# Kernel optimization log

Measured on AMD Instinct MI355X. Metric: run time of the kernel, lower is better.

The kernel has to match this reference:

```python
import jax, jax.numpy as jnp
import numpy as np

EMB = 512       # emb_dim
H = 8           # n_heads
HD = EMB // H   # head_dim = 64
FREQ = 64       # freq_features
PERIOD = 0.1
N = 2048


def setup_inputs() -> dict:
    key = jax.random.key(0)
    ks = jax.random.split(key, 6)
    x = jax.random.normal(ks[0], (1, N, EMB), dtype=jnp.float32)
    v = jax.random.normal(ks[1], (1, N, 3), dtype=jnp.float32)
    vec_map = v / jnp.linalg.norm(v, axis=-1, keepdims=True)  # unit direction vectors
    s_in = 1.0 / np.sqrt(EMB)
    W_qkv = jax.random.normal(ks[2], (EMB, 3 * EMB), dtype=jnp.float32) * s_in
    b_qkv = jnp.zeros((3 * EMB,), dtype=jnp.float32)
    W_bias = jax.random.normal(ks[3], (FREQ, H), dtype=jnp.float32) * (1.0 / np.sqrt(FREQ))
    b_bias = jnp.zeros((H,), dtype=jnp.float32)
    W_out = jax.random.normal(ks[4], (EMB, EMB), dtype=jnp.float32) * s_in
    b_out = jnp.zeros((EMB,), dtype=jnp.float32)
    return {"x": x, "vec_map": vec_map, "W_qkv": W_qkv, "b_qkv": b_qkv,
            "W_bias": W_bias, "b_bias": b_bias, "W_out": W_out, "b_out": b_out}


def reference(x, vec_map, W_qkv, b_qkv, W_bias, b_bias, W_out, b_out):
    batch_dim = x.shape[:-2]
    n = x.shape[-2]
    # QKV projection -> (*, N, H, 3, HD)
    qkv = (x @ W_qkv + b_qkv).reshape(*batch_dim, n, H, 3, HD)
    q, k, v = (qkv[..., 0, :], qkv[..., 1, :], qkv[..., 2, :])
    # attention scores (*, Q, K, H), softmax over the K axis (axis=-2)
    attn = jnp.einsum('...qht,...kht->...qkh', q, k) / np.sqrt(HD)
    attn = jax.nn.softmax(attn, axis=-2)
    # relative bias from pairwise angles between direction vectors
    dot = jnp.einsum('...nc,...mc->...nm', vec_map, vec_map)
    angle = jnp.arccos(jnp.clip(dot, 0.0, 1.0)) / 0.001
    freqs = jnp.linspace(0.0, 1.0, FREQ // 2, dtype=jnp.float32) / PERIOD
    phase = freqs * angle[..., None]                      # (*, N, N, FREQ/2)
    pos = jnp.concatenate((jnp.sin(phase), jnp.cos(phase)), axis=-1)  # (*, N, N, FREQ)
    bias = pos @ W_bias + b_bias                          # (*, N, N, H)
    attn = attn + bias
    # weighted sum of values -> (*, N, EMB)
    y = jnp.einsum('...qkh,...kht->...qht', attn, v).reshape(*batch_dim, n, EMB)
    return y @ W_out + b_out
```

## Files before the change

### kernel.cpp

```cpp
#include <hip/hip_runtime.h>
#include <hip/hip_bf16.h>
#include <math.h>

#define NT 2048
#define EMBD 512
#define NH 8
#define QKV_LD 1536

typedef unsigned short u16;
typedef __attribute__((ext_vector_type(8))) short short8;
typedef __attribute__((ext_vector_type(4))) float v4f;

static __device__ __forceinline__ float bf2f(unsigned int u) {
    union { unsigned int i; float f; } c; c.i = u << 16; return c.f;
}
static __device__ __forceinline__ void unpack4(uint2 r, float* f) {
    f[0] = bf2f(r.x & 0xffffu); f[1] = bf2f(r.x >> 16);
    f[2] = bf2f(r.y & 0xffffu); f[3] = bf2f(r.y >> 16);
}
static __device__ __forceinline__ unsigned int f2bf(float x) {
    union { float f; unsigned int u; } c; c.f = x;
    return (c.u + 0x7fffu + ((c.u >> 16) & 1u)) >> 16;
}

__global__ __launch_bounds__(256) void split_x(const float* __restrict__ x,
    u16* __restrict__ xh, u16* __restrict__ xl)
{
    int i = (blockIdx.x * 256 + threadIdx.x) << 2;
    float4 v = *(const float4*)(x + i);
    float f[4] = {v.x, v.y, v.z, v.w};
    unsigned int hi[4], lo[4];
#pragma unroll
    for (int j = 0; j < 4; ++j) {
        hi[j] = f2bf(f[j]);
        lo[j] = f2bf(f[j] - bf2f(hi[j]));
    }
    uint2 wh; wh.x = hi[0] | (hi[1] << 16); wh.y = hi[2] | (hi[3] << 16);
    uint2 wl; wl.x = lo[0] | (lo[1] << 16); wl.y = lo[2] | (lo[3] << 16);
    *(uint2*)(xh + i) = wh;
    *(uint2*)(xl + i) = wl;
}

__global__ __launch_bounds__(256) void split_wt(const float* __restrict__ W,
    u16* __restrict__ wth, u16* __restrict__ wtl, int ld)
{
    __shared__ float tile[64][65];
    const int n0 = blockIdx.x << 6, k0 = blockIdx.y << 6;
    const int t = threadIdx.x;
    const int r = t >> 2, c4 = (t & 3) << 4;
#pragma unroll
    for (int j = 0; j < 4; ++j)
        *(float4*)&tile[r][c4 + (j << 2)] =
            *(const float4*)(W + (size_t)(k0 + r) * ld + n0 + c4 + (j << 2));
    __syncthreads();
    const int n_l = t >> 2;
    u16 th[16], tl[16];
#pragma unroll
    for (int j = 0; j < 16; ++j) {
        float f = tile[c4 + j][n_l];
        unsigned int h = f2bf(f);
        th[j] = (u16)h;
        tl[j] = (u16)f2bf(f - bf2f(h));
    }
    u16* dh = wth + (size_t)(n0 + n_l) * EMBD + k0 + c4;
    u16* dl = wtl + (size_t)(n0 + n_l) * EMBD + k0 + c4;
    *(uint4*)dh       = *(uint4*)&th[0];
    *(uint4*)(dh + 8) = *(uint4*)&th[8];
    *(uint4*)dl       = *(uint4*)&tl[0];
    *(uint4*)(dl + 8) = *(uint4*)&tl[8];
}

__global__ __launch_bounds__(256) void gemm_qkv_mfma(const u16* __restrict__ xh,
    const u16* __restrict__ xl, const u16* __restrict__ wth,
    const u16* __restrict__ wtl, const float* __restrict__ bias,
    u16* __restrict__ qkvb)
{
    const int n0 = blockIdx.x << 6, m0 = blockIdx.y << 6;
    const int w = threadIdx.x >> 6, lane = threadIdx.x & 63;
    const int wm = w >> 1, wn = w & 1;
    const int fr = lane & 15, kd = (lane >> 4) << 3;

    const u16* ah0 = xh + (size_t)(m0 + wm * 32 + fr) * EMBD + kd;
    const u16* al0 = xl + (size_t)(m0 + wm * 32 + fr) * EMBD + kd;
    const u16* bh0 = wth + (size_t)(n0 + wn * 32 + fr) * EMBD + kd;
    const u16* bl0 = wtl + (size_t)(n0 + wn * 32 + fr) * EMBD + kd;

    v4f acc[2][2] = {};
    for (int kc = 0; kc < EMBD; kc += 32) {
        short8 a_h[2], a_l[2], b_h[2], b_l[2];
#pragma unroll
        for (int im = 0; im < 2; ++im) {
            a_h[im] = *(const short8*)(ah0 + (size_t)im * 16 * EMBD + kc);
            a_l[im] = *(const short8*)(al0 + (size_t)im * 16 * EMBD + kc);
        }
#pragma unroll
        for (int in = 0; in < 2; ++in) {
            b_h[in] = *(const short8*)(bh0 + (size_t)in * 16 * EMBD + kc);
            b_l[in] = *(const short8*)(bl0 + (size_t)in * 16 * EMBD + kc);
        }
#pragma unroll
        for (int im = 0; im < 2; ++im)
#pragma unroll
            for (int in = 0; in < 2; ++in) {
                acc[im][in] = __builtin_amdgcn_mfma_f32_16x16x32_bf16(a_h[im], b_h[in], acc[im][in], 0, 0, 0);
                acc[im][in] = __builtin_amdgcn_mfma_f32_16x16x32_bf16(a_h[im], b_l[in], acc[im][in], 0, 0, 0);
                acc[im][in] = __builtin_amdgcn_mfma_f32_16x16x32_bf16(a_l[im], b_h[in], acc[im][in], 0, 0, 0);
            }
    }
    const int qr = (lane >> 4) << 2;
#pragma unroll
    for (int im = 0; im < 2; ++im)
#pragma unroll
        for (int in = 0; in < 2; ++in) {
            int n = n0 + wn * 32 + in * 16 + fr;
            float bv = bias[n];
#pragma unroll
            for (int r = 0; r < 4; ++r) {
                int m = m0 + wm * 32 + im * 16 + qr + r;
                qkvb[(size_t)m * QKV_LD + n] = (u16)f2bf(acc[im][in][r] + bv);
            }
        }
}

__global__ __launch_bounds__(256) void transpose_v(const u16* __restrict__ qkvb,
                                                   u16* __restrict__ Vt)
{
    __shared__ u16 tile[64][72];
    const int h = blockIdx.y, k0 = blockIdx.x << 6;
    const int t = threadIdx.x;
    {
        int r = t >> 2, cg = (t & 3) << 4;
        const u16* src = qkvb + (size_t)(k0 + r) * QKV_LD + h * 192 + 128 + cg;
        *(uint4*)&tile[r][cg]     = *(const uint4*)src;
        *(uint4*)&tile[r][cg + 8] = *(const uint4*)(src + 8);
    }
    __syncthreads();
    {
        int c = t >> 2, kg = (t & 3) << 4;
        u16 tmp[16];
#pragma unroll
        for (int j = 0; j < 16; ++j) tmp[j] = tile[kg + j][c];
        u16* dst = Vt + ((size_t)h * 64 + c) * NT + k0 + kg;
        *(uint4*)dst       = *(uint4*)&tmp[0];
        *(uint4*)(dst + 8) = *(uint4*)&tmp[8];
    }
}

__global__ __launch_bounds__(256) void scores_mfma(const u16* __restrict__ qkvb,
                                                   u16* __restrict__ s,
                                                   float* __restrict__ zbuf)
{
    __shared__ u16 tile[128][144];
    const int h = blockIdx.z;
    const int kb = blockIdx.x << 7;
    const int qb = blockIdx.y << 7;
    const int w = threadIdx.x >> 6;
    const int q0 = qb + (w << 5);
    const int lane = threadIdx.x & 63;
    const int fr = lane & 15;
    const int kd = (lane >> 4) << 3;

    const u16* qbase = qkvb + (size_t)(q0 + fr) * QKV_LD + h * 192 + kd;
    const u16* kbase = qkvb + (size_t)(kb + fr) * QKV_LD + h * 192 + 64 + kd;

    short8 aq[2][2];
    aq[0][0] = *(const short8*)(qbase);
    aq[0][1] = *(const short8*)(qbase + 32);
    aq[1][0] = *(const short8*)(qbase + (size_t)16 * QKV_LD);
    aq[1][1] = *(const short8*)(qbase + (size_t)16 * QKV_LD + 32);

    v4f acc[2][8] = {};
#pragma unroll
    for (int nt = 0; nt < 8; ++nt) {
        short8 b0 = *(const short8*)(kbase + (size_t)nt * 16 * QKV_LD);
        short8 b1 = *(const short8*)(kbase + (size_t)nt * 16 * QKV_LD + 32);
        acc[0][nt] = __builtin_amdgcn_mfma_f32_16x16x32_bf16(aq[0][0], b0, acc[0][nt], 0, 0, 0);
        acc[0][nt] = __builtin_amdgcn_mfma_f32_16x16x32_bf16(aq[0][1], b1, acc[0][nt], 0, 0, 0);
        acc[1][nt] = __builtin_amdgcn_mfma_f32_16x16x32_bf16(aq[1][0], b0, acc[1][nt], 0, 0, 0);
        acc[1][nt] = __builtin_amdgcn_mfma_f32_16x16x32_bf16(aq[1][1], b1, acc[1][nt], 0, 0, 0);
    }
    const int qr = (lane >> 4) << 2;
#pragma unroll
    for (int i = 0; i < 2; ++i)
#pragma unroll
        for (int nt = 0; nt < 8; ++nt)
#pragma unroll
            for (int r = 0; r < 4; ++r)
                tile[(w << 5) + (i << 4) + qr + r][(nt << 4) + fr] =
                    (u16)f2bf(acc[i][nt][r] * 0.125f);
    float es[2][4];
#pragma unroll
    for (int i = 0; i < 2; ++i)
#pragma unroll
        for (int r = 0; r < 4; ++r) {
            float sum = 0.f;
#pragma unroll
            for (int nt = 0; nt < 8; ++nt)
                sum += __expf(acc[i][nt][r] * 0.125f);
            es[i][r] = sum;
        }
#pragma unroll
    for (int off = 1; off < 16; off <<= 1)
#pragma unroll
        for (int i = 0; i < 2; ++i)
#pragma unroll
            for (int r = 0; r < 4; ++r)
                es[i][r] += __shfl_xor(es[i][r], off);
    if (fr == 0) {
#pragma unroll
        for (int i = 0; i < 2; ++i)
#pragma unroll
            for (int r = 0; r < 4; ++r)
                atomicAdd(zbuf + h * NT + q0 + (i << 4) + qr + r, es[i][r]);
    }
    __syncthreads();
    const int row0 = threadIdx.x >> 4;
    const int col = (threadIdx.x & 15) << 3;
#pragma unroll
    for (int l = 0; l < 8; ++l) {
        int row = row0 + (l << 4);
        *(uint4*)(s + ((size_t)h * NT + qb + row) * NT + kb + col) =
            *(uint4*)&tile[row][col];
    }
}

__global__ __launch_bounds__(256) void bias_kernel(u16* __restrict__ s,
    const float* __restrict__ vec, const float* __restrict__ Wb,
    const float* __restrict__ bb, const float* __restrict__ zbuf)
{
    __shared__ float flds[32];
    __shared__ float vql[96], vkl[96];
    __shared__ float bbl[8];
    __shared__ float ang_lds[1057];
    __shared__ float biasl[8 * 1057];

    const int t = threadIdx.x;
    int b = blockIdx.x, tq = 0, rem = 64;
    while (b >= rem) { b -= rem; ++tq; --rem; }
    const int tk = tq + b;
    const int q0 = tq << 5, k0 = tk << 5;

    if (t < 32) flds[t] = __fdiv_rn(__fdiv_rn((float)t, 31.0f), 0.1f);
    else if (t < 128) vql[t - 32] = vec[q0 * 3 + (t - 32)];
    else if (t < 224) vkl[t - 128] = vec[k0 * 3 + (t - 128)];
    else if (t < 232) bbl[t - 224] = bb[t - 224];
    __syncthreads();

    {
        const int qq = t & 31, kb = (t >> 5) << 2;
        const float a0 = vql[qq * 3], a1 = vql[qq * 3 + 1], a2 = vql[qq * 3 + 2];
#pragma unroll
        for (int j = 0; j < 4; ++j) {
            const int kk = kb + j;
            float c0 = vkl[kk * 3], c1 = vkl[kk * 3 + 1], c2 = vkl[kk * 3 + 2];
            float dot = __fadd_rn(__fadd_rn(__fmul_rn(a0, c0), __fmul_rn(a1, c1)),
                                  __fmul_rn(a2, c2));
            float dotc = fminf(fmaxf(dot, 0.0f), 1.0f);
            ang_lds[qq * 33 + kk] = __fdiv_rn(acosf(dotc), 0.001f);
        }
    }
    __syncthreads();

    {
        const int w = t >> 6, lane = t & 63;
        const int fr = lane & 15, kd = (lane >> 4) << 3, qr = (lane >> 4) << 2;
        short8 BS, BC;
#pragma unroll
        for (int j = 0; j < 8; ++j) {
            float ws = (fr < 8) ? Wb[(kd + j) * 8 + fr] : 0.0f;
            float wc = (fr < 8) ? Wb[(32 + kd + j) * 8 + fr] : 0.0f;
            BS[j] = (short)f2bf(ws);
            BC[j] = (short)f2bf(wc);
        }
        for (int tt = w; tt < 64; tt += 4) {
            int p = (tt << 4) + fr;
            float ang = ang_lds[(p >> 5) * 33 + (p & 31)];
            short8 AS, AC;
#pragma unroll
            for (int j = 0; j < 8; ++j) {
                float ph = __fmul_rn(flds[kd + j], ang);
                float rv = ph * 0.15915494309189535f;
                float rf = rv - floorf(rv);
                AS[j] = (short)f2bf(__builtin_amdgcn_sinf(rf));
                AC[j] = (short)f2bf(__builtin_amdgcn_cosf(rf));
            }
            v4f c = {};
            c = __builtin_amdgcn_mfma_f32_16x16x32_bf16(AS, BS, c, 0, 0, 0);
            c = __builtin_amdgcn_mfma_f32_16x16x32_bf16(AC, BC, c, 0, 0, 0);
            if (fr < 8) {
#pragma unroll
                for (int r = 0; r < 4; ++r) {
                    int pp = (tt << 4) + qr + r;
                    biasl[fr * 1057 + (pp >> 5) * 33 + (pp & 31)] = c[r];
                }
            }
        }
    }
    __syncthreads();

    const int r = t >> 3;
    const int cg = (t & 7) << 2;
    {
        const int q = q0 + r;
#pragma unroll
        for (int h = 0; h < 8; ++h) {
            const float iz = 1.0f / zbuf[h * NT + q];
            const float bv = bbl[h];
            const size_t base = ((size_t)h * NT + q) * NT + k0 + cg;
            uint2 raw = *(const uint2*)(s + base);
            float v[4]; unpack4(raw, v);
            unsigned int o[4];
#pragma unroll
            for (int j = 0; j < 4; ++j) {
                float bias = biasl[h * 1057 + r * 33 + cg + j];
                o[j] = f2bf(__expf(v[j]) * iz + bias + bv);
            }
            uint2 wv; wv.x = o[0] | (o[1] << 16); wv.y = o[2] | (o[3] << 16);
            *(uint2*)(s + base) = wv;
        }
    }
    if (tk != tq) {
        const int q = k0 + r;
#pragma unroll
        for (int h = 0; h < 8; ++h) {
            const float iz = 1.0f / zbuf[h * NT + q];
            const float bv = bbl[h];
            const size_t base = ((size_t)h * NT + q) * NT + q0 + cg;
            uint2 raw = *(const uint2*)(s + base);
            float v[4]; unpack4(raw, v);
            unsigned int o[4];
#pragma unroll
            for (int j = 0; j < 4; ++j) {
                float bias = biasl[h * 1057 + (cg + j) * 33 + r];
                o[j] = f2bf(__expf(v[j]) * iz + bias + bv);
            }
            uint2 wv; wv.x = o[0] | (o[1] << 16); wv.y = o[2] | (o[3] << 16);
            *(uint2*)(s + base) = wv;
        }
    }
}

__global__ __launch_bounds__(256) void attnv_mfma(const u16* __restrict__ attn,
    const u16* __restrict__ Vt, float* __restrict__ ypart)
{
    const int h = blockIdx.y, z = blockIdx.z;
    const int q0 = (blockIdx.x << 6) + ((threadIdx.x >> 6) << 4);
    const int lane = threadIdx.x & 63;
    const int fr = lane & 15;
    const int kd = (lane >> 4) << 3;
    const int kbase = z << 9;

    const u16* arow  = attn + (size_t)(h * NT + q0 + fr) * NT + kbase + kd;
    const u16* vbase = Vt + ((size_t)h * 64 + fr) * NT + kbase + kd;

    v4f c[4] = {};
    for (int ks = 0; ks < 512; ks += 32) {
        short8 a = *(const short8*)(arow + ks);
#pragma unroll
        for (int nt = 0; nt < 4; ++nt) {
            short8 bv = *(const short8*)(vbase + (size_t)nt * 16 * NT + ks);
            c[nt] = __builtin_amdgcn_mfma_f32_16x16x32_bf16(a, bv, c[nt], 0, 0, 0);
        }
    }
    float* yp = ypart + (size_t)z * NT * EMBD;
    const int qr = (lane >> 4) << 2;
#pragma unroll
    for (int nt = 0; nt < 4; ++nt)
#pragma unroll
        for (int r = 0; r < 4; ++r)
            yp[(size_t)(q0 + qr + r) * EMBD + (h << 6) + (nt << 4) + fr] = c[nt][r];
}

__global__ __launch_bounds__(256) void reduce_y(const float* __restrict__ parts,
    u16* __restrict__ yh, u16* __restrict__ yl)
{
    const int MN = NT * EMBD;
    int i = (blockIdx.x * 256 + threadIdx.x) << 2;
    float4 acc = *(const float4*)(parts + i);
#pragma unroll
    for (int sp = 1; sp < 4; ++sp) {
        float4 p = *(const float4*)(parts + (size_t)sp * MN + i);
        acc.x += p.x; acc.y += p.y; acc.z += p.z; acc.w += p.w;
    }
    float f[4] = {acc.x, acc.y, acc.z, acc.w};
    unsigned int hi[4], lo[4];
#pragma unroll
    for (int j = 0; j < 4; ++j) {
        hi[j] = f2bf(f[j]);
        lo[j] = f2bf(f[j] - bf2f(hi[j]));
    }
    uint2 wh; wh.x = hi[0] | (hi[1] << 16); wh.y = hi[2] | (hi[3] << 16);
    uint2 wl; wl.x = lo[0] | (lo[1] << 16); wl.y = lo[2] | (lo[3] << 16);
    *(uint2*)(yh + i) = wh;
    *(uint2*)(yl + i) = wl;
}

__global__ __launch_bounds__(256) void gemm_out_mfma(const u16* __restrict__ yh,
    const u16* __restrict__ yl, const u16* __restrict__ wh,
    const u16* __restrict__ wl, const float* __restrict__ bias,
    float* __restrict__ out)
{
    const int n0 = blockIdx.x << 6, m0 = blockIdx.y << 6;
    const int w = threadIdx.x >> 6, lane = threadIdx.x & 63;
    const int wm = w >> 1, wn = w & 1;
    const int fr = lane & 15, kd = (lane >> 4) << 3;

    const u16* ah0 = yh + (size_t)(m0 + wm * 32 + fr) * EMBD + kd;
    const u16* al0 = yl + (size_t)(m0 + wm * 32 + fr) * EMBD + kd;
    const u16* bh0 = wh + (size_t)(n0 + wn * 32 + fr) * EMBD + kd;
    const u16* bl0 = wl + (size_t)(n0 + wn * 32 + fr) * EMBD + kd;

    v4f acc[2][2] = {};
    for (int kc = 0; kc < EMBD; kc += 32) {
        short8 a_h[2], a_l[2], b_h[2], b_l[2];
#pragma unroll
        for (int im = 0; im < 2; ++im) {
            a_h[im] = *(const short8*)(ah0 + (size_t)im * 16 * EMBD + kc);
            a_l[im] = *(const short8*)(al0 + (size_t)im * 16 * EMBD + kc);
        }
#pragma unroll
        for (int in = 0; in < 2; ++in) {
            b_h[in] = *(const short8*)(bh0 + (size_t)in * 16 * EMBD + kc);
            b_l[in] = *(const short8*)(bl0 + (size_t)in * 16 * EMBD + kc);
        }
#pragma unroll
        for (int im = 0; im < 2; ++im)
#pragma unroll
            for (int in = 0; in < 2; ++in) {
                acc[im][in] = __builtin_amdgcn_mfma_f32_16x16x32_bf16(a_h[im], b_h[in], acc[im][in], 0, 0, 0);
                acc[im][in] = __builtin_amdgcn_mfma_f32_16x16x32_bf16(a_h[im], b_l[in], acc[im][in], 0, 0, 0);
                acc[im][in] = __builtin_amdgcn_mfma_f32_16x16x32_bf16(a_l[im], b_h[in], acc[im][in], 0, 0, 0);
            }
    }
    const int qr = (lane >> 4) << 2;
#pragma unroll
    for (int im = 0; im < 2; ++im)
#pragma unroll
        for (int in = 0; in < 2; ++in) {
            int n = n0 + wn * 32 + in * 16 + fr;
            float bv = bias[n];
#pragma unroll
            for (int r = 0; r < 4; ++r) {
                int m = m0 + wm * 32 + im * 16 + qr + r;
                out[(size_t)m * EMBD + n] = acc[im][in][r] + bv;
            }
        }
}

extern "C" void kernel_launch(void* const* d_in, const int* in_sizes, int n_in,
                              void* d_out, int out_size, void* d_ws, size_t ws_size,
                              hipStream_t stream)
{
    const float* x    = (const float*)d_in[0];
    const float* vec  = (const float*)d_in[1];
    const float* Wqkv = (const float*)d_in[2];
    const float* bqkv = (const float*)d_in[3];
    const float* Wb   = (const float*)d_in[4];
    const float* bb   = (const float*)d_in[5];
    const float* Wout = (const float*)d_in[6];
    const float* bout = (const float*)d_in[7];
    float* out = (float*)d_out;

    char* ws = (char*)d_ws;
    u16*   qkvb  = (u16*)(ws);
    u16*   sbuf  = (u16*)(ws + 6291456);
    u16*   Vt    = (u16*)(ws + 73400320);
    float* zbuf  = (float*)(ws + 75497472);
    u16*   yh    = (u16*)(ws + 75628544);
    u16*   yl    = (u16*)(ws + 77725696);
    float* parts = (float*)(ws + 79822848);
    u16*   xh    = (u16*)(ws + 79822848);
    u16*   xl    = (u16*)(ws + 81920000);
    u16*   wth   = (u16*)(ws + 84017152);
    u16*   wtl   = (u16*)(ws + 85590016);
    u16*   woth  = (u16*)(ws + 79822848);
    u16*   wotl  = (u16*)(ws + 80347136);

    hipMemsetAsync(zbuf, 0, NH * NT * sizeof(float), stream);
    split_x<<<1024, 256, 0, stream>>>(x, xh, xl);
    split_wt<<<dim3(24, 8), 256, 0, stream>>>(Wqkv, wth, wtl, QKV_LD);
    gemm_qkv_mfma<<<dim3(24, 32), 256, 0, stream>>>(xh, xl, wth, wtl, bqkv, qkvb);
    transpose_v<<<dim3(32, 8), 256, 0, stream>>>(qkvb, Vt);
    scores_mfma<<<dim3(16, 16, 8), 256, 0, stream>>>(qkvb, sbuf, zbuf);
    bias_kernel<<<2080, 256, 0, stream>>>(sbuf, vec, Wb, bb, zbuf);
    attnv_mfma<<<dim3(32, 8, 4), 256, 0, stream>>>(sbuf, Vt, parts);
    reduce_y<<<1024, 256, 0, stream>>>(parts, yh, yl);
    split_wt<<<dim3(8, 8), 256, 0, stream>>>(Wout, woth, wotl, EMBD);
    gemm_out_mfma<<<dim3(8, 32), 256, 0, stream>>>(yh, yl, woth, wotl, bout, out);
}
```

Baseline: 273.6 us.

## Fuse scores, bias and attn@V into one flash-style kernel without materializing NxN

Replaces the separate scores, bias and attn·V kernels, which wrote and reread a bf16 H×N×N score buffer, with one fused kernel. For each 32-query tile and K-split it computes QK^T, exp, the angle-based bias via MFMA, and multiplies both exp-scores and bias by V in registers. It keeps two partial accumulators (unnormalized P·V and bias·V) plus partial row sums, and a reduce kernel normalizes and combines them. This removes the large global round-trips and the memset, but the launch is only 256 blocks of 512 threads, which may leave the GPU underoccupied. It also recomputes the bias for every query/key pair instead of exploiting symmetry.

```diff
diff --git a/kernel.cpp b/kernel.cpp
--- a/kernel.cpp
+++ b/kernel.cpp
@@ -6,6 +6,7 @@
 #define EMBD 512
 #define NH 8
 #define QKV_LD 1536
+#define KSPLIT 4
 
 typedef unsigned short u16;
 typedef __attribute__((ext_vector_type(8))) short short8;
@@ -13,10 +14,6 @@
 
 static __device__ __forceinline__ float bf2f(unsigned int u) {
     union { unsigned int i; float f; } c; c.i = u << 16; return c.f;
-}
-static __device__ __forceinline__ void unpack4(uint2 r, float* f) {
-    f[0] = bf2f(r.x & 0xffffu); f[1] = bf2f(r.x >> 16);
-    f[2] = bf2f(r.y & 0xffffu); f[3] = bf2f(r.y >> 16);
 }
 static __device__ __forceinline__ unsigned int f2bf(float x) {
     union { float f; unsigned int u; } c; c.f = x;
@@ -146,243 +143,226 @@
     }
 }
 
-__global__ __launch_bounds__(256) void scores_mfma(const u16* __restrict__ qkvb,
-                                                   u16* __restrict__ s,
-                                                   float* __restrict__ zbuf)
-{
-    __shared__ u16 tile[128][144];
-    const int h = blockIdx.z;
-    const int kb = blockIdx.x << 7;
-    const int qb = blockIdx.y << 7;
-    const int w = threadIdx.x >> 6;
-    const int q0 = qb + (w << 5);
-    const int lane = threadIdx.x & 63;
+__global__ __launch_bounds__(512, 2) void fused_attn(
+    const u16* __restrict__ qkvb, const u16* __restrict__ Vt,
+    const float* __restrict__ vec, const float* __restrict__ Wb,
+    const float* __restrict__ bb, float* __restrict__ zpart,
+    float* __restrict__ partsP, float* __restrict__ partsB)
+{
+    __shared__ float flds[32];
+    __shared__ float vql[96];
+    __shared__ float ang[32 * 65];
+    __shared__ u16 tile[8 * 2056];
+
+    const int bid = blockIdx.x;
+    const int xcd = bid & 7;
+    const int zsp = xcd >> 1;
+    const int qt  = ((bid >> 3) << 1) | (xcd & 1);
+    const int q0 = qt << 5;
+    const int kbase = zsp << 9;
+
+    const int t = threadIdx.x;
+    const int w = t >> 6;
+    const int lane = t & 63;
     const int fr = lane & 15;
-    const int kd = (lane >> 4) << 3;
-
-    const u16* qbase = qkvb + (size_t)(q0 + fr) * QKV_LD + h * 192 + kd;
-    const u16* kbase = qkvb + (size_t)(kb + fr) * QKV_LD + h * 192 + 64 + kd;
-
-    short8 aq[2][2];
-    aq[0][0] = *(const short8*)(qbase);
-    aq[0][1] = *(const short8*)(qbase + 32);
-    aq[1][0] = *(const short8*)(qbase + (size_t)16 * QKV_LD);
-    aq[1][1] = *(const short8*)(qbase + (size_t)16 * QKV_LD + 32);
-
-    v4f acc[2][8] = {};
-#pragma unroll
-    for (int nt = 0; nt < 8; ++nt) {
-        short8 b0 = *(const short8*)(kbase + (size_t)nt * 16 * QKV_LD);
-        short8 b1 = *(const short8*)(kbase + (size_t)nt * 16 * QKV_LD + 32);
-        acc[0][nt] = __builtin_amdgcn_mfma_f32_16x16x32_bf16(aq[0][0], b0, acc[0][nt], 0, 0, 0);
-        acc[0][nt] = __builtin_amdgcn_mfma_f32_16x16x32_bf16(aq[0][1], b1, acc[0][nt], 0, 0, 0);
-        acc[1][nt] = __builtin_amdgcn_mfma_f32_16x16x32_bf16(aq[1][0], b0, acc[1][nt], 0, 0, 0);
-        acc[1][nt] = __builtin_amdgcn_mfma_f32_16x16x32_bf16(aq[1][1], b1, acc[1][nt], 0, 0, 0);
-    }
-    const int qr = (lane >> 4) << 2;
-#pragma unroll
-    for (int i = 0; i < 2; ++i)
-#pragma unroll
-        for (int nt = 0; nt < 8; ++nt)
-#pragma unroll
-            for (int r = 0; r < 4; ++r)
-                tile[(w << 5) + (i << 4) + qr + r][(nt << 4) + fr] =
-                    (u16)f2bf(acc[i][nt][r] * 0.125f);
-    float es[2][4];
-#pragma unroll
-    for (int i = 0; i < 2; ++i)
-#pragma unroll
-        for (int r = 0; r < 4; ++r) {
-            float sum = 0.f;
-#pragma unroll
-            for (int nt = 0; nt < 8; ++nt)
-                sum += __expf(acc[i][nt][r] * 0.125f);
-            es[i][r] = sum;
-        }
-#pragma unroll
-    for (int off = 1; off < 16; off <<= 1)
-#pragma unroll
-        for (int i = 0; i < 2; ++i)
-#pragma unroll
-            for (int r = 0; r < 4; ++r)
-                es[i][r] += __shfl_xor(es[i][r], off);
-    if (fr == 0) {
-#pragma unroll
-        for (int i = 0; i < 2; ++i)
-#pragma unroll
-            for (int r = 0; r < 4; ++r)
-                atomicAdd(zbuf + h * NT + q0 + (i << 4) + qr + r, es[i][r]);
-    }
-    __syncthreads();
-    const int row0 = threadIdx.x >> 4;
-    const int col = (threadIdx.x & 15) << 3;
-#pragma unroll
-    for (int l = 0; l < 8; ++l) {
-        int row = row0 + (l << 4);
-        *(uint4*)(s + ((size_t)h * NT + qb + row) * NT + kb + col) =
-            *(uint4*)&tile[row][col];
-    }
-}
-
-__global__ __launch_bounds__(256) void bias_kernel(u16* __restrict__ s,
-    const float* __restrict__ vec, const float* __restrict__ Wb,
-    const float* __restrict__ bb, const float* __restrict__ zbuf)
-{
-    __shared__ float flds[32];
-    __shared__ float vql[96], vkl[96];
-    __shared__ float bbl[8];
-    __shared__ float ang_lds[1057];
-    __shared__ float biasl[8 * 1057];
-
-    const int t = threadIdx.x;
-    int b = blockIdx.x, tq = 0, rem = 64;
-    while (b >= rem) { b -= rem; ++tq; --rem; }
-    const int tk = tq + b;
-    const int q0 = tq << 5, k0 = tk << 5;
+    const int hi4 = lane >> 4;
+    const int kd = hi4 << 3;
+    const int qr = hi4 << 2;
 
     if (t < 32) flds[t] = __fdiv_rn(__fdiv_rn((float)t, 31.0f), 0.1f);
     else if (t < 128) vql[t - 32] = vec[q0 * 3 + (t - 32)];
-    else if (t < 224) vkl[t - 128] = vec[k0 * 3 + (t - 128)];
-    else if (t < 232) bbl[t - 224] = bb[t - 224];
+
+    short8 BS, BC;
+#pragma unroll
+    for (int j = 0; j < 8; ++j) {
+        float ws = (fr < 8) ? Wb[(kd + j) * 8 + fr] : 0.0f;
+        float wc = (fr < 8) ? Wb[(32 + kd + j) * 8 + fr] : 0.0f;
+        BS[j] = (short)f2bf(ws);
+        BC[j] = (short)f2bf(wc);
+    }
+    const float bbv = (fr < 8) ? bb[fr] : 0.0f;
+
+    short8 aq[2][2];
+#pragma unroll
+    for (int mb = 0; mb < 2; ++mb)
+#pragma unroll
+        for (int kk = 0; kk < 2; ++kk)
+            aq[mb][kk] = *(const short8*)(qkvb +
+                (size_t)(q0 + mb * 16 + fr) * QKV_LD + w * 192 + kk * 32 + kd);
+
+    v4f accP[2][4] = {};
+    v4f accB[2][4] = {};
+    float zacc[2][4] = {};
+
     __syncthreads();
 
-    {
-        const int qq = t & 31, kb = (t >> 5) << 2;
-        const float a0 = vql[qq * 3], a1 = vql[qq * 3 + 1], a2 = vql[qq * 3 + 2];
-#pragma unroll
-        for (int j = 0; j < 4; ++j) {
-            const int kk = kb + j;
-            float c0 = vkl[kk * 3], c1 = vkl[kk * 3 + 1], c2 = vkl[kk * 3 + 2];
-            float dot = __fadd_rn(__fadd_rn(__fmul_rn(a0, c0), __fmul_rn(a1, c1)),
-                                  __fmul_rn(a2, c2));
-            float dotc = fminf(fmaxf(dot, 0.0f), 1.0f);
-            ang_lds[qq * 33 + kk] = __fdiv_rn(acosf(dotc), 0.001f);
-        }
-    }
-    __syncthreads();
-
-    {
-        const int w = t >> 6, lane = t & 63;
-        const int fr = lane & 15, kd = (lane >> 4) << 3, qr = (lane >> 4) << 2;
-        short8 BS, BC;
-#pragma unroll
-        for (int j = 0; j < 8; ++j) {
-            float ws = (fr < 8) ? Wb[(kd + j) * 8 + fr] : 0.0f;
-            float wc = (fr < 8) ? Wb[(32 + kd + j) * 8 + fr] : 0.0f;
-            BS[j] = (short)f2bf(ws);
-            BC[j] = (short)f2bf(wc);
-        }
-        for (int tt = w; tt < 64; tt += 4) {
-            int p = (tt << 4) + fr;
-            float ang = ang_lds[(p >> 5) * 33 + (p & 31)];
+    for (int c = 0; c < 8; ++c) {
+        const int kc = kbase + (c << 6);
+        {
+            const int p0 = t << 2;
+            const int q = p0 >> 6;
+            const int kl = p0 & 63;
+            const float a0 = vql[q * 3], a1 = vql[q * 3 + 1], a2 = vql[q * 3 + 2];
+            const float* vk = vec + (size_t)(kc + kl) * 3;
+#pragma unroll
+            for (int j = 0; j < 4; ++j) {
+                float c0 = vk[j * 3], c1 = vk[j * 3 + 1], c2 = vk[j * 3 + 2];
+                float dot = __fadd_rn(__fadd_rn(__fmul_rn(a0, c0), __fmul_rn(a1, c1)),
+                                      __fmul_rn(a2, c2));
+                float dotc = fminf(fmaxf(dot, 0.0f), 1.0f);
+                ang[q * 65 + kl + j] = __fdiv_rn(acosf(dotc), 0.001f);
+            }
+        }
+        __syncthreads();
+#pragma unroll
+        for (int gi = 0; gi < 16; ++gi) {
+            const int g = w + (gi << 3);
+            const int q = g >> 2;
+            const int ksub = (g & 3) << 4;
+            const float av = ang[q * 65 + ksub + fr];
             short8 AS, AC;
 #pragma unroll
             for (int j = 0; j < 8; ++j) {
-                float ph = __fmul_rn(flds[kd + j], ang);
+                float ph = __fmul_rn(flds[kd + j], av);
                 float rv = ph * 0.15915494309189535f;
                 float rf = rv - floorf(rv);
                 AS[j] = (short)f2bf(__builtin_amdgcn_sinf(rf));
                 AC[j] = (short)f2bf(__builtin_amdgcn_cosf(rf));
             }
-            v4f c = {};
-            c = __builtin_amdgcn_mfma_f32_16x16x32_bf16(AS, BS, c, 0, 0, 0);
-            c = __builtin_amdgcn_mfma_f32_16x16x32_bf16(AC, BC, c, 0, 0, 0);
+            v4f cb = {};
+            cb = __builtin_amdgcn_mfma_f32_16x16x32_bf16(AS, BS, cb, 0, 0, 0);
+            cb = __builtin_amdgcn_mfma_f32_16x16x32_bf16(AC, BC, cb, 0, 0, 0);
             if (fr < 8) {
+                const int kg = (ksub + qr) >> 3;
+                unsigned int pk0 = f2bf(cb[0] + bbv) | (f2bf(cb[1] + bbv) << 16);
+                unsigned int pk1 = f2bf(cb[2] + bbv) | (f2bf(cb[3] + bbv) << 16);
+                uint2 wv; wv.x = pk0; wv.y = pk1;
+                *(uint2*)&tile[fr * 2056 + q * 64 + ((kg ^ (q & 7)) << 3) + (qr & 7)] = wv;
+            }
+        }
+        __syncthreads();
+        short8 vb[4][2], bk[4][2];
+#pragma unroll
+        for (int nt = 0; nt < 4; ++nt)
+#pragma unroll
+            for (int kk = 0; kk < 2; ++kk) {
+                vb[nt][kk] = *(const short8*)(Vt +
+                    (size_t)(w * 64 + nt * 16 + fr) * NT + kc + kk * 32 + kd);
+                bk[nt][kk] = *(const short8*)(qkvb +
+                    (size_t)(kc + nt * 16 + fr) * QKV_LD + w * 192 + 64 + kk * 32 + kd);
+            }
+#pragma unroll
+        for (int mb = 0; mb < 2; ++mb) {
+            const int q = mb * 16 + fr;
+#pragma unroll
+            for (int kk = 0; kk < 2; ++kk) {
+                short8 ab = *(const short8*)&tile[w * 2056 + q * 64 +
+                    (((kk * 4 + hi4) ^ (q & 7)) << 3)];
+#pragma unroll
+                for (int nt = 0; nt < 4; ++nt)
+                    accB[mb][nt] = __builtin_amdgcn_mfma_f32_16x16x32_bf16(ab, vb[nt][kk], accB[mb][nt], 0, 0, 0);
+            }
+        }
+        v4f sacc[2][4] = {};
+#pragma unroll
+        for (int mb = 0; mb < 2; ++mb)
+#pragma unroll
+            for (int nt = 0; nt < 4; ++nt) {
+                sacc[mb][nt] = __builtin_amdgcn_mfma_f32_16x16x32_bf16(aq[mb][0], bk[nt][0], sacc[mb][nt], 0, 0, 0);
+                sacc[mb][nt] = __builtin_amdgcn_mfma_f32_16x16x32_bf16(aq[mb][1], bk[nt][1], sacc[mb][nt], 0, 0, 0);
+            }
+        unsigned int pk[2][4][2];
+#pragma unroll
+        for (int mb = 0; mb < 2; ++mb)
+#pragma unroll
+            for (int nt = 0; nt < 4; ++nt)
+#pragma unroll
+                for (int r2 = 0; r2 < 2; ++r2) {
+                    float e0 = __expf(sacc[mb][nt][2 * r2] * 0.125f);
+                    float e1 = __expf(sacc[mb][nt][2 * r2 + 1] * 0.125f);
+                    zacc[mb][2 * r2] += e0;
+                    zacc[mb][2 * r2 + 1] += e1;
+                    pk[mb][nt][r2] = f2bf(e0) | (f2bf(e1) << 16);
+                }
+        __syncthreads();
+#pragma unroll
+        for (int mb = 0; mb < 2; ++mb)
+#pragma unroll
+            for (int nt = 0; nt < 4; ++nt) {
+                const int kg = (nt << 1) + (fr >> 3);
 #pragma unroll
                 for (int r = 0; r < 4; ++r) {
-                    int pp = (tt << 4) + qr + r;
-                    biasl[fr * 1057 + (pp >> 5) * 33 + (pp & 31)] = c[r];
+                    const int q = mb * 16 + qr + r;
+                    tile[w * 2056 + q * 64 + ((kg ^ (q & 7)) << 3) + (fr & 7)] =
+                        (u16)(pk[mb][nt][r >> 1] >> ((r & 1) << 4));
                 }
             }
-        }
-    }
-    __syncthreads();
-
-    const int r = t >> 3;
-    const int cg = (t & 7) << 2;
-    {
-        const int q = q0 + r;
-#pragma unroll
-        for (int h = 0; h < 8; ++h) {
-            const float iz = 1.0f / zbuf[h * NT + q];
-            const float bv = bbl[h];
-            const size_t base = ((size_t)h * NT + q) * NT + k0 + cg;
-            uint2 raw = *(const uint2*)(s + base);
-            float v[4]; unpack4(raw, v);
-            unsigned int o[4];
-#pragma unroll
-            for (int j = 0; j < 4; ++j) {
-                float bias = biasl[h * 1057 + r * 33 + cg + j];
-                o[j] = f2bf(__expf(v[j]) * iz + bias + bv);
-            }
-            uint2 wv; wv.x = o[0] | (o[1] << 16); wv.y = o[2] | (o[3] << 16);
-            *(uint2*)(s + base) = wv;
-        }
-    }
-    if (tk != tq) {
-        const int q = k0 + r;
-#pragma unroll
-        for (int h = 0; h < 8; ++h) {
-            const float iz = 1.0f / zbuf[h * NT + q];
-            const float bv = bbl[h];
-            const size_t base = ((size_t)h * NT + q) * NT + q0 + cg;
-            uint2 raw = *(const uint2*)(s + base);
-            float v[4]; unpack4(raw, v);
-            unsigned int o[4];
-#pragma unroll
-            for (int j = 0; j < 4; ++j) {
-                float bias = biasl[h * 1057 + (cg + j) * 33 + r];
-                o[j] = f2bf(__expf(v[j]) * iz + bias + bv);
-            }
-            uint2 wv; wv.x = o[0] | (o[1] << 16); wv.y = o[2] | (o[3] << 16);
-            *(uint2*)(s + base) = wv;
-        }
-    }
-}
-
-__global__ __launch_bounds__(256) void attnv_mfma(const u16* __restrict__ attn,
-    const u16* __restrict__ Vt, float* __restrict__ ypart)
-{
-    const int h = blockIdx.y, z = blockIdx.z;
-    const int q0 = (blockIdx.x << 6) + ((threadIdx.x >> 6) << 4);
-    const int lane = threadIdx.x & 63;
-    const int fr = lane & 15;
-    const int kd = (lane >> 4) << 3;
-    const int kbase = z << 9;
-
-    const u16* arow  = attn + (size_t)(h * NT + q0 + fr) * NT + kbase + kd;
-    const u16* vbase = Vt + ((size_t)h * 64 + fr) * NT + kbase + kd;
-
-    v4f c[4] = {};
-    for (int ks = 0; ks < 512; ks += 32) {
-        short8 a = *(const short8*)(arow + ks);
-#pragma unroll
-        for (int nt = 0; nt < 4; ++nt) {
-            short8 bv = *(const short8*)(vbase + (size_t)nt * 16 * NT + ks);
-            c[nt] = __builtin_amdgcn_mfma_f32_16x16x32_bf16(a, bv, c[nt], 0, 0, 0);
-        }
-    }
-    float* yp = ypart + (size_t)z * NT * EMBD;
-    const int qr = (lane >> 4) << 2;
-#pragma unroll
-    for (int nt = 0; nt < 4; ++nt)
-#pragma unroll
-        for (int r = 0; r < 4; ++r)
-            yp[(size_t)(q0 + qr + r) * EMBD + (h << 6) + (nt << 4) + fr] = c[nt][r];
-}
-
-__global__ __launch_bounds__(256) void reduce_y(const float* __restrict__ parts,
+        __syncthreads();
+#pragma unroll
+        for (int mb = 0; mb < 2; ++mb) {
+            const int q = mb * 16 + fr;
+#pragma unroll
+            for (int kk = 0; kk < 2; ++kk) {
+                short8 ap = *(const short8*)&tile[w * 2056 + q * 64 +
+                    (((kk * 4 + hi4) ^ (q & 7)) << 3)];
+#pragma unroll
+                for (int nt = 0; nt < 4; ++nt)
+                    accP[mb][nt] = __builtin_amdgcn_mfma_f32_16x16x32_bf16(ap, vb[nt][kk], accP[mb][nt], 0, 0, 0);
+            }
+        }
+    }
+#pragma unroll
+    for (int off = 1; off < 16; off <<= 1)
+#pragma unroll
+        for (int mb = 0; mb < 2; ++mb)
+#pragma unroll
+            for (int r = 0; r < 4; ++r)
+                zacc[mb][r] += __shfl_xor(zacc[mb][r], off);
+    if (fr == 0) {
+#pragma unroll
+        for (int mb = 0; mb < 2; ++mb)
+#pragma unroll
+            for (int r = 0; r < 4; ++r)
+                zpart[((size_t)zsp * 8 + w) * NT + q0 + mb * 16 + qr + r] = zacc[mb][r];
+    }
+    float* pP = partsP + (size_t)zsp * NT * EMBD;
+    float* pB = partsB + (size_t)zsp * NT * EMBD;
+#pragma unroll
+    for (int mb = 0; mb < 2; ++mb)
+#pragma unroll
+        for (int nt = 0; nt < 4; ++nt)
+#pragma unroll
+            for (int r = 0; r < 4; ++r) {
+                const size_t idx = (size_t)(q0 + mb * 16 + qr + r) * EMBD +
+                                   (w << 6) + (nt << 4) + fr;
+                pP[idx] = accP[mb][nt][r];
+                pB[idx] = accB[mb][nt][r];
+            }
+}
+
+__global__ __launch_bounds__(256) void reduce_y2(const float* __restrict__ partsP,
+    const float* __restrict__ partsB, const float* __restrict__ zpart,
     u16* __restrict__ yh, u16* __restrict__ yl)
 {
     const int MN = NT * EMBD;
     int i = (blockIdx.x * 256 + threadIdx.x) << 2;
-    float4 acc = *(const float4*)(parts + i);
-#pragma unroll
-    for (int sp = 1; sp < 4; ++sp) {
-        float4 p = *(const float4*)(parts + (size_t)sp * MN + i);
-        acc.x += p.x; acc.y += p.y; acc.z += p.z; acc.w += p.w;
-    }
-    float f[4] = {acc.x, acc.y, acc.z, acc.w};
+    const int q = i >> 9;
+    const int h = (i & 511) >> 6;
+    float zs = 0.0f;
+#pragma unroll
+    for (int z = 0; z < KSPLIT; ++z) zs += zpart[((size_t)z * 8 + h) * NT + q];
+    float4 aP = *(const float4*)(partsP + i);
+    float4 aB = *(const float4*)(partsB + i);
+#pragma unroll
+    for (int z = 1; z < KSPLIT; ++z) {
+        float4 p = *(const float4*)(partsP + (size_t)z * MN + i);
+        float4 b = *(const float4*)(partsB + (size_t)z * MN + i);
+        aP.x += p.x; aP.y += p.y; aP.z += p.z; aP.w += p.w;
+        aB.x += b.x; aB.y += b.y; aB.z += b.z; aB.w += b.w;
+    }
+    const float iz = 1.0f / zs;
+    float f[4] = {aP.x * iz + aB.x, aP.y * iz + aB.y,
+                  aP.z * iz + aB.z, aP.w * iz + aB.w};
     unsigned int hi[4], lo[4];
 #pragma unroll
     for (int j = 0; j < 4; ++j) {
@@ -462,29 +442,27 @@
     float* out = (float*)d_out;
 
     char* ws = (char*)d_ws;
-    u16*   qkvb  = (u16*)(ws);
-    u16*   sbuf  = (u16*)(ws + 6291456);
-    u16*   Vt    = (u16*)(ws + 73400320);
-    float* zbuf  = (float*)(ws + 75497472);
-    u16*   yh    = (u16*)(ws + 75628544);
-    u16*   yl    = (u16*)(ws + 77725696);
-    float* parts = (float*)(ws + 79822848);
-    u16*   xh    = (u16*)(ws + 79822848);
-    u16*   xl    = (u16*)(ws + 81920000);
-    u16*   wth   = (u16*)(ws + 84017152);
-    u16*   wtl   = (u16*)(ws + 85590016);
-    u16*   woth  = (u16*)(ws + 79822848);
-    u16*   wotl  = (u16*)(ws + 80347136);
-
-    hipMemsetAsync(zbuf, 0, NH * NT * sizeof(float), stream);
+    u16*   qkvb   = (u16*)(ws);
+    u16*   Vt     = (u16*)(ws + 6291456);
+    float* zpart  = (float*)(ws + 8388608);
+    float* partsP = (float*)(ws + 8650752);
+    float* partsB = (float*)(ws + 25427968);
+    u16*   yh     = (u16*)(ws + 42205184);
+    u16*   yl     = (u16*)(ws + 44302336);
+    u16*   xh     = (u16*)(ws + 46399488);
+    u16*   xl     = (u16*)(ws + 48496640);
+    u16*   wth    = (u16*)(ws + 50593792);
+    u16*   wtl    = (u16*)(ws + 52166656);
+    u16*   woth   = (u16*)(ws + 46399488);
+    u16*   wotl   = (u16*)(ws + 46923776);
+
     split_x<<<1024, 256, 0, stream>>>(x, xh, xl);
     split_wt<<<dim3(24, 8), 256, 0, stream>>>(Wqkv, wth, wtl, QKV_LD);
     gemm_qkv_mfma<<<dim3(24, 32), 256, 0, stream>>>(xh, xl, wth, wtl, bqkv, qkvb);
     transpose_v<<<dim3(32, 8), 256, 0, stream>>>(qkvb, Vt);
-    scores_mfma<<<dim3(16, 16, 8), 256, 0, stream>>>(qkvb, sbuf, zbuf);
-    bias_kernel<<<2080, 256, 0, stream>>>(sbuf, vec, Wb, bb, zbuf);
-    attnv_mfma<<<dim3(32, 8, 4), 256, 0, stream>>>(sbuf, Vt, parts);
-    reduce_y<<<1024, 256, 0, stream>>>(parts, yh, yl);
+    fused_attn<<<64 * KSPLIT, 512, 0, stream>>>(qkvb, Vt, vec, Wb, bb,
+                                                zpart, partsP, partsB);
+    reduce_y2<<<1024, 256, 0, stream>>>(partsP, partsB, zpart, yh, yl);
     split_wt<<<dim3(8, 8), 256, 0, stream>>>(Wout, woth, wotl, EMBD);
     gemm_out_mfma<<<dim3(8, 32), 256, 0, stream>>>(yh, yl, woth, wotl, bout, out);
 }
```

Result: faster. 264.9 us (-3.2%).
